# Kernel tuning notes

Measured on AMD Instinct MI355X. Metric: run time of the kernel, lower is better.

## Reference

```python
import jax, jax.numpy as jnp
import numpy as np
from jax.scipy.special import i0

# NUFFT adjoint (gridding) configuration, matching m_op.plan(uv, (256,256), (512,512), (6,6))
N = 256          # image side
K = 512
J = 6            # kernel support per dim
B = 8            # batch
M = 100000       # n_measurements
ALPHA = K / N    # oversampling = 2
BETA = float(np.pi * np.sqrt((J / ALPHA * (ALPHA - 0.5)) ** 2 - 0.8))  # Fessler KB beta


def setup_inputs() -> dict:
    key = jax.random.key(0)
    k1, k2, k3, k4 = jax.random.split(key, 4)
    y_real = jax.random.normal(k1, (B, M), dtype=jnp.float32)
    y_imag = jax.random.normal(k2, (B, M), dtype=jnp.float32)
    weights = jax.random.uniform(k3, (M,), dtype=jnp.float32, minval=0.1, maxval=1.0)
    uv = jax.random.uniform(k4, (M, 2), dtype=jnp.float32,
                            minval=-np.pi, maxval=np.pi)
    return {"y_real": y_real, "y_imag": y_imag, "weights": weights, "uv": uv}


def _kb(t):
    # Kaiser-Bessel interpolation kernel, support |t| <= J/2
    u = 2.0 * t / J
    return i0(BETA * jnp.sqrt(jnp.clip(1.0 - u * u, 0.0))) / i0(jnp.asarray(BETA, jnp.float32))


def reference(y_real, y_imag, weights, uv):
    # weighted complex measurements: inputs * measurement_weights
    y = (y_real + 1j * y_imag) * weights[None, :]           # (B, M) complex64

    # map uv in [-pi, pi) to oversampled grid coords in [0, K)
    kf = uv * (K / (2.0 * np.pi))                            # (M, 2), DC at index 0 (mod K)
    base = jnp.floor(kf).astype(jnp.int32)                   # (M, 2)
    offs = jnp.arange(-J // 2 + 1, J // 2 + 1)               # [-2..3], 6 taps
    idx = base[:, :, None] + offs[None, None, :]             # (M, 2, J)
    dist = idx.astype(jnp.float32) - kf[:, :, None]
    w = _kb(dist)                                            # (M, 2, J) separable weights
    idxm = jnp.mod(idx, K)                                   # wrap onto torus

    w2 = (w[:, 0, :, None] * w[:, 1, None, :]).reshape(M, J * J)          # (M, 36)
    lin = (idxm[:, 0, :, None] * K + idxm[:, 1, None, :]).reshape(M * J * J)
    vals = (y[:, :, None] * w2[None, :, :].astype(jnp.complex64)).reshape(B, M * J * J)

    # scatter-add onto oversampled Fourier grid
    grid = jnp.zeros((B, K * K), jnp.complex64).at[:, lin].add(vals)
    grid = grid.reshape(B, K, K)

    # inverse FFT, center, crop to N x N
    img = jnp.fft.fftshift(jnp.fft.ifft2(grid), axes=(1, 2))
    c = K // 2
    img = img[:, c - N // 2:c + N // 2, c - N // 2:c + N // 2]

    # deapodization: divide by 1D FT of the KB kernel (always real here since BETA > pi*J/4*... )
    n = jnp.arange(N, dtype=jnp.float32) - N // 2
    xf = np.pi * J * n / K
    arg = BETA * BETA - xf * xf
    d = jnp.sinh(jnp.sqrt(arg)) / jnp.sqrt(arg)              # (N,)
    apod = d[:, None] * d[None, :]

    x = (jnp.real(img) / apod).astype(jnp.float32)           # tf.math.real(adj_op(...))

    # per-image min-max rescale
    tmax = jnp.max(x, axis=(1, 2), keepdims=True)
    tmin = jnp.min(x, axis=(1, 2), keepdims=True)
    return (x - tmin) / (tmax - tmin)
```

## Files before the change

### kernel.cpp

```cpp
#include <hip/hip_runtime.h>
#include <math.h>

#define NN 256
#define KK 512
#define JJ 6
#define BB 8
#define MPTS 100000
#define NBINS (KK * KK)
#define KF_SCALE 81.48733086305615f

typedef _Float16 h8 __attribute__((ext_vector_type(8)));
typedef _Float16 h2 __attribute__((ext_vector_type(2)));


__device__ __forceinline__ float i0f_dev(float x) {
    float ax = fabsf(x);
    if (ax < 3.75f) {
        float t = x / 3.75f; t *= t;
        return 1.0f + t*(3.5156229f + t*(3.0899424f + t*(1.2067492f +
               t*(0.2659732f + t*(0.0360768f + t*0.0045813f)))));
    } else {
        float t = 3.75f / ax;
        return (expf(ax) * rsqrtf(ax)) *
               (0.39894228f + t*(0.01328592f + t*(0.00225319f + t*(-0.00157565f +
                t*(0.00916281f + t*(-0.02057706f + t*(0.02635537f +
                t*(-0.01647633f + t*0.00392377f))))))));
    }
}

__device__ __forceinline__ float kbf(float t, float beta, float inv_i0b) {
    float u = t * (1.0f / 3.0f);
    float q = fmaxf(1.0f - u * u, 0.0f);
    return i0f_dev(beta * sqrtf(q)) * inv_i0b;
}

__device__ __forceinline__ int wave_scan(int x, int lane) {
#pragma unroll
    for (int off = 1; off < 64; off <<= 1) {
        int y = __shfl_up(x, off, 64);
        if (lane >= off) x += y;
    }
    return x;
}

__device__ __forceinline__ float kb_lut(const float* __restrict__ sT, float t) {
    float u = (t + 3.0f) * (1023.0f / 6.0f);
    int i = (int)u;
    i = min(i, 1022);
    float f = u - (float)i;
    float a = sT[i];
    return a + f * (sT[i + 1] - sT[i]);
}

__device__ __forceinline__ void tw_lookup(const float* __restrict__ twc,
                                          const float* __restrict__ tws,
                                          int idx, float& wr, float& wi) {
    float sg = (idx & 256) ? -1.0f : 1.0f;
    int ib = idx & 255;
    wr = sg * twc[ib];
    wi = sg * tws[ib];
}


__device__ __forceinline__ void fill_point(
    const float2* __restrict__ uv2,
    const float* __restrict__ y_real, const float* __restrict__ y_imag,
    const float* __restrict__ weights, const int* __restrict__ offsets,
    int* counts, char* rec, const float* sT, int m)
{
    float2 u = uv2[m];
    float kf0 = u.x * KF_SCALE;
    float kf1 = u.y * KF_SCALE;
    float f0 = floorf(kf0), f1 = floorf(kf1);
    float fr0 = kf0 - f0, fr1 = kf1 - f1;
    int b1c = (int)f1 & (KK - 1);
    int bin = (((int)f0 & (KK - 1)) << 9) | b1c;
    int old = atomicSub(&counts[bin], 1);
    int slot = offsets[bin] + old - 1;

    _Float16 hw[12];
#pragma unroll
    for (int j = 0; j < JJ; ++j) {
        hw[j]     = (_Float16)kb_lut(sT, (float)(j - 2) - fr0);
        hw[6 + j] = (_Float16)kb_lut(sT, (float)(j - 2) - fr1);
    }

    float4 c0v, c1v;
    _Float16* p0 = (_Float16*)&c0v;
    _Float16* p1 = (_Float16*)&c1v;
#pragma unroll
    for (int j = 0; j < 8; ++j) p0[j] = hw[j];
#pragma unroll
    for (int j = 0; j < 4; ++j) p1[j] = hw[8 + j];
    ((int*)&c1v)[2] = b1c;
    ((int*)&c1v)[3] = 0;

    float wm = weights[m];
    h8 ha, hb;
#pragma unroll
    for (int b = 0; b < 4; ++b) {
        ha[2 * b]     = (_Float16)(y_real[b * MPTS + m] * wm);
        ha[2 * b + 1] = (_Float16)(y_imag[b * MPTS + m] * wm);
        hb[2 * b]     = (_Float16)(y_real[(b + 4) * MPTS + m] * wm);
        hb[2 * b + 1] = (_Float16)(y_imag[(b + 4) * MPTS + m] * wm);
    }

    float4* dst = (float4*)(rec + (size_t)slot * 64);
    dst[0] = c0v;
    dst[1] = c1v;
    dst[2] = *(float4*)&ha;
    dst[3] = *(float4*)&hb;
}

__device__ __forceinline__ void gather_strip(
    const int* __restrict__ offsets, const char* __restrict__ rec,
    h2* __restrict__ gridh, char* myl, int j, int w, int lane)
{
    int half = lane >> 5;
    int l32 = lane & 31;
    int xcd = j & 7;
    int c0 = (xcd << 6) + ((j >> 3) & 63);
    int q4 = j >> 9;
    int c1base = (q4 << 7) + (w << 5);
    int c1 = c1base + l32;
    int wa = c1 - 3, wb = c1 + 2;

    float aR[4], aI[4];
#pragma unroll
    for (int b = 0; b < 4; ++b) { aR[b] = 0.0f; aI[b] = 0.0f; }

    for (int j0 = 0; j0 < JJ; ++j0) {
        int r0 = (c0 - (j0 - 2)) & (KK - 1);
        int rowbase = r0 << 9;
        int lo = c1base - 3, hi = c1base + 33;
        int nseg, ga0, gb0, ga1, gb1;
        if (lo < 0)        { ga0 = lo; gb0 = -1;  ga1 = 0;   gb1 = hi; nseg = 2; }
        else if (hi > 511) { ga0 = lo; gb0 = 511; ga1 = 512; gb1 = hi; nseg = 2; }
        else               { ga0 = lo; gb0 = hi;  ga1 = 0;   gb1 = 0;  nseg = 1; }

        for (int sgi = 0; sgi < nseg; ++sgi) {
            int ga = sgi ? ga1 : ga0;
            int gb = sgi ? gb1 : gb0;
            int pstart = offsets[rowbase + (ga & 511)];
            int pend   = offsets[rowbase + ((gb & 511) + 1)];
            int ia = max(wa, ga), ib = min(wb, gb);
            bool has = ia <= ib;
            int pA = has ? offsets[rowbase + (ia & 511)] : 0;
            int pB = has ? ((ib == gb) ? pend
                                       : offsets[rowbase + ((ib + 1) & 511)]) : 0;

            for (int pc = pstart; pc < pend; pc += 32) {
                int cnt = min(32, pend - pc);
                int sub = lane & 3;
                int prow = lane >> 2;
#pragma unroll
                for (int qq = 0; qq < 2; ++qq) {
                    if (16 * qq < cnt) {
                        int pp = min(pc + prow + 16 * qq, MPTS - 1);
                        float4 v = *(const float4*)(rec + (size_t)pp * 64 + sub * 16);
                        *(float4*)(myl + (prow + 16 * qq) * 88 + sub * 16) = v;
                    }
                }
                int pLo = max(pA, pc), pHi = min(pB, pc + cnt);
                for (int p = pLo; p < pHi; ++p) {
                    const char* rp = myl + (p - pc) * 88;
                    int bin1 = *(const int*)(rp + 24);
                    int idx = (c1 - bin1 + 2) & 511;
                    bool ok = idx <= 5;
                    idx = ok ? idx : 0;
                    float w0 = (float)*(const _Float16*)(rp + j0 * 2);
                    float w1 = (float)*(const _Float16*)(rp + 12 + idx * 2);
                    float ww = ok ? w0 * w1 : 0.0f;
                    h8 yv = *(const h8*)(rp + 32 + (half << 4));
#pragma unroll
                    for (int b = 0; b < 4; ++b) {
                        aR[b] += (float)yv[2 * b]     * ww;
                        aI[b] += (float)yv[2 * b + 1] * ww;
                    }
                }
            }
        }
    }

    int c = (c0 << 9) + c1;
#pragma unroll
    for (int b = 0; b < 4; ++b) {
        h2 v;
        v[0] = (_Float16)aR[b];
        v[1] = (_Float16)aI[b];
        gridh[((size_t)((half << 2) + b) << 18) + c] = v;
    }
}

__device__ __forceinline__ void wave_fft512(float xr[8], float xi[8], int lane,
                                            const float* __restrict__ twc,
                                            const float* __restrict__ tws)
{
    float a0r = xr[0]+xr[4], a0i = xi[0]+xi[4];
    float a4r = xr[0]-xr[4], a4i = xi[0]-xi[4];
    float a2r = xr[2]+xr[6], a2i = xi[2]+xi[6];
    float a6r = xr[2]-xr[6], a6i = xi[2]-xi[6];
    float a1r = xr[1]+xr[5], a1i = xi[1]+xi[5];
    float a5r = xr[1]-xr[5], a5i = xi[1]-xi[5];
    float a3r = xr[3]+xr[7], a3i = xi[3]+xi[7];
    float a7r = xr[3]-xr[7], a7i = xi[3]-xi[7];
    float b0r = a0r+a2r, b0i = a0i+a2i;
    float b2r = a0r-a2r, b2i = a0i-a2i;
    float b4r = a4r-a6i, b4i = a4i+a6r;
    float b6r = a4r+a6i, b6i = a4i-a6r;
    float b1r = a1r+a3r, b1i = a1i+a3i;
    float b3r = a1r-a3r, b3i = a1i-a3i;
    float b5r = a5r-a7i, b5i = a5i+a7r;
    float b7r = a5r+a7i, b7i = a5i-a7r;
    const float S2 = 0.70710678118654752f;
    float w5r = S2*(b5r-b5i), w5i = S2*(b5r+b5i);
    float w7r = -S2*(b7r+b7i), w7i = S2*(b7r-b7i);
    float y1r = b4r+w5r, y1i = b4i+w5i;
    float y5r = b4r-w5r, y5i = b4i-w5i;
    float y2r = b2r-b3i, y2i = b2i+b3r;
    float y6r = b2r+b3i, y6i = b2i-b3r;
    float y3r = b6r+w7r, y3i = b6i+w7i;
    float y7r = b6r-w7r, y7i = b6i-w7i;

    int p = __brev((unsigned)lane) >> 26;
    xr[0] = b0r+b1r; xi[0] = b0i+b1i;
    {
        float wr, wi;
        tw_lookup(twc, tws, p,     wr, wi); xr[1] = y1r*wr - y1i*wi; xi[1] = y1i*wr + y1r*wi;
        tw_lookup(twc, tws, p * 2, wr, wi); xr[2] = y2r*wr - y2i*wi; xi[2] = y2i*wr + y2r*wi;
        tw_lookup(twc, tws, p * 3, wr, wi); xr[3] = y3r*wr - y3i*wi; xi[3] = y3i*wr + y3r*wi;
        float y4r = b0r-b1r, y4i = b0i-b1i;
        tw_lookup(twc, tws, p * 4, wr, wi); xr[4] = y4r*wr - y4i*wi; xi[4] = y4i*wr + y4r*wi;
        tw_lookup(twc, tws, p * 5, wr, wi); xr[5] = y5r*wr - y5i*wi; xi[5] = y5i*wr + y5r*wi;
        tw_lookup(twc, tws, p * 6, wr, wi); xr[6] = y6r*wr - y6i*wi; xi[6] = y6i*wr + y6r*wi;
        tw_lookup(twc, tws, p * 7, wr, wi); xr[7] = y7r*wr - y7i*wi; xi[7] = y7i*wr + y7r*wi;
    }

#pragma unroll
    for (int t = 0; t < 6; ++t) {
        int m = 1 << t;
        int j = lane & (m - 1);
        int ti = j << (8 - t);
        float wc = twc[ti], wsn = tws[ti];
        bool hi = (lane & m) != 0;
#pragma unroll
        for (int d = 0; d < 8; ++d) {
            float pR = __shfl_xor(xr[d], m, 64);
            float pI = __shfl_xor(xi[d], m, 64);
            float bR = hi ? xr[d] : pR;
            float bI = hi ? xi[d] : pI;
            float aR = hi ? pR : xr[d];
            float aI = hi ? pI : xi[d];
            float wbR = wc * bR - wsn * bI;
            float wbI = wc * bI + wsn * bR;
            xr[d] = hi ? aR - wbR : aR + wbR;
            xi[d] = hi ? aI - wbI : aI + wbI;
        }
    }
}

__device__ __forceinline__ void wave_fft256(float xr[4], float xi[4], int lane,
                                            const float* __restrict__ twc,
                                            const float* __restrict__ tws)
{
    float t0r = xr[0]+xr[2], t0i = xi[0]+xi[2];
    float t1r = xr[0]-xr[2], t1i = xi[0]-xi[2];
    float t2r = xr[1]+xr[3], t2i = xi[1]+xi[3];
    float t3r = xr[1]-xr[3], t3i = xi[1]-xi[3];
    float y1r = t1r-t3i, y1i = t1i+t3r;
    float y3r = t1r+t3i, y3i = t1i-t3r;

    int p2 = (__brev((unsigned)lane) >> 26) << 1;
    xr[0] = t0r+t2r; xi[0] = t0i+t2i;
    {
        float wr, wi;
        tw_lookup(twc, tws, p2,     wr, wi); xr[1] = y1r*wr - y1i*wi; xi[1] = y1i*wr + y1r*wi;
        float y2r = t0r-t2r, y2i = t0i-t2i;
        tw_lookup(twc, tws, p2 * 2, wr, wi); xr[2] = y2r*wr - y2i*wi; xi[2] = y2i*wr + y2r*wi;
        tw_lookup(twc, tws, p2 * 3, wr, wi); xr[3] = y3r*wr - y3i*wi; xi[3] = y3i*wr + y3r*wi;
    }

#pragma unroll
    for (int t = 0; t < 6; ++t) {
        int m = 1 << t;
        int j = lane & (m - 1);
        int ti = j << (8 - t);
        float wc = twc[ti], wsn = tws[ti];
        bool hi = (lane & m) != 0;
#pragma unroll
        for (int d = 0; d < 4; ++d) {
            float pR = __shfl_xor(xr[d], m, 64);
            float pI = __shfl_xor(xi[d], m, 64);
            float bR = hi ? xr[d] : pR;
            float bI = hi ? xi[d] : pI;
            float aR = hi ? pR : xr[d];
            float aI = hi ? pI : xi[d];
            float wbR = wc * bR - wsn * bI;
            float wbI = wc * bI + wsn * bR;
            xr[d] = hi ? aR - wbR : aR + wbR;
            xi[d] = hi ? aI - wbI : aI + wbI;
        }
    }
}

__device__ __forceinline__ void fftA_body(const h2* __restrict__ gridh,
                                          h2* __restrict__ Ch, int bx, int t,
                                          float* sR, float* sI,
                                          float* twc, float* tws)
{
    int lane = t & 63;
    int w = t >> 6;
    int x  = bx & 7;
    int b  = (bx >> 3) & 7;
    int k1base = (x << 6) | (((bx >> 6) & 7) << 3);
    int k1 = k1base + w;

    if (t < 256) {
        float ang = (float)(2.0 * M_PI / 512.0) * (float)t;
        float s, c; sincosf(ang, &s, &c);
        twc[t] = c; tws[t] = s;
    }

    const h2* row = gridh + ((size_t)b << 18) + ((size_t)k1 << 9);
    int p = __brev((unsigned)lane) >> 26;
    float xr[8], xi[8];
#pragma unroll
    for (int a = 0; a < 8; ++a) {
        h2 v = row[p + (a << 6)];
        xr[a] = (float)v[0]; xi[a] = (float)v[1];
    }
    __syncthreads();

    wave_fft512(xr, xi, lane, twc, tws);

    bool act = (lane < 16) | (lane >= 48);
    int lpp = (lane < 16) ? lane : (lane - 32);
    if (act) {
#pragma unroll
        for (int d = 0; d < 8; ++d) {
            int addr = w * 264 + d * 33 + lpp;
            sR[addr] = xr[d];
            sI[addr] = xi[d];
        }
    }
    __syncthreads();

#pragma unroll
    for (int pp = 0; pp < 4; ++pp) {
        int idx = pp * 512 + t;
        int kk = idx & 7;
        int s2 = idx >> 3;
        int v = (s2 + 128) & 255;
        int d = v & 7;
        int lp = v >> 3;
        int addr = kk * 264 + d * 33 + lp;
        h2 o;
        o[0] = (_Float16)sR[addr];
        o[1] = (_Float16)sI[addr];
        Ch[(((size_t)(b << 8) + s2) << 9) + k1base + kk] = o;
    }
}

__device__ __forceinline__ void fftB_body(const h2* __restrict__ Ch,
                                          float* __restrict__ imgT, float beta2,
                                          float* __restrict__ pmin,
                                          float* __restrict__ pmax,
                                          int bx, int t,
                                          float* twc, float* tws, float* invd,
                                          float (*wor)[256], float* wmn, float* wmx)
{
    int lane = t & 63;
    int w = t >> 6;
    int row = w >> 1;
    int odd = w & 1;
    int rowid = bx * 4 + row;
    int b = rowid >> 8;
    int s2 = rowid & 255;

    if (t < 256) {
        float ang = (float)(2.0 * M_PI / 512.0) * (float)t;
        float s, c; sincosf(ang, &s, &c);
        twc[t] = c; tws[t] = s;
    } else if (t < 512) {
        int i = t - 256;
        const float XF = (float)(M_PI * (double)JJ / (double)KK);
        float n = (float)(i - 128);
        float xf = XF * n;
        float arg = beta2 - xf * xf;
        float sq = sqrtf(arg);
        invd[i] = sq / sinhf(sq);
    }

    const h2* rowp = Ch + ((size_t)rowid << 9);
    int p = __brev((unsigned)lane) >> 26;
    float xr[4], xi[4];
#pragma unroll
    for (int a = 0; a < 4; ++a) {
        h2 v = rowp[((p + (a << 6)) << 1) | odd];
        xr[a] = (float)v[0]; xi[a] = (float)v[1];
    }
    __syncthreads();

    wave_fft256(xr, xi, lane, twc, tws);

    if (odd) {
        float4 wo;
#pragma unroll
        for (int d = 0; d < 4; ++d) {
            int k = (lane << 2) + d;
            ((float*)&wo)[d] = xr[d] * twc[k] - xi[d] * tws[k];
        }
        *(float4*)&wor[row][lane << 2] = wo;
    }
    __syncthreads();

    if (!odd) {
        const float INVK2 = 1.0f / ((float)KK * (float)KK);
        float sbase = INVK2 * invd[s2];
        float lmin = 1e30f, lmax = -1e30f;
        float4 wo = *(const float4*)&wor[row][lane << 2];
        float vals[4];
#pragma unroll
        for (int d = 0; d < 4; ++d) {
            int k = (lane << 2) + d;
            float e = xr[d];
            float woK = ((const float*)&wo)[d];
            float xre = (k < 128) ? (e + woK) : (e - woK);
            int r = (k + 128) & 255;
            float o = xre * sbase * invd[r];
            vals[d] = o;
            lmin = fminf(lmin, o);
            lmax = fmaxf(lmax, o);
        }
        int r0run = ((lane << 2) + 128) & 255;
        *(float4*)(imgT + ((size_t)b << 16) + (s2 << 8) + r0run) =
            make_float4(vals[0], vals[1], vals[2], vals[3]);
#pragma unroll
        for (int off = 32; off >= 1; off >>= 1) {
            lmin = fminf(lmin, __shfl_xor(lmin, off, 64));
            lmax = fmaxf(lmax, __shfl_xor(lmax, off, 64));
        }
        if (lane == 0) { wmn[row] = lmin; wmx[row] = lmax; }
    }
    __syncthreads();
    if (t == 0) {
        float mn = fminf(fminf(wmn[0], wmn[1]), fminf(wmn[2], wmn[3]));
        float mx = fmaxf(fmaxf(wmx[0], wmx[1]), fmaxf(wmx[2], wmx[3]));
        pmin[bx] = mn;
        pmax[bx] = mx;
    }
}

__device__ __forceinline__ void norm_body(const float* __restrict__ imgT,
                                          const float* __restrict__ pmin,
                                          const float* __restrict__ pmax,
                                          float* __restrict__ out,
                                          int bx, int t, int nthr,
                                          float (*tile)[65], float* s_mn, float* s_inv)
{
    int b = bx >> 4;
    int tl = bx & 15;
    int r0 = (tl & 3) << 6;
    int s0 = (tl >> 2) << 6;
    int tr = t & 63;
    int ts = t >> 6;
    int nts = nthr >> 6;

    if (t < 64) {
        float mn = pmin[(b << 6) + t];
        float mx = pmax[(b << 6) + t];
#pragma unroll
        for (int off = 32; off >= 1; off >>= 1) {
            mn = fminf(mn, __shfl_xor(mn, off, 64));
            mx = fmaxf(mx, __shfl_xor(mx, off, 64));
        }
        if (t == 0) { *s_mn = mn; *s_inv = 1.0f / (mx - mn); }
    }

    const float* src = imgT + ((size_t)b << 16);
    for (int s2i = ts; s2i < 64; s2i += nts)
        tile[s2i][tr] = src[((s0 + s2i) << 8) + r0 + tr];
    __syncthreads();

    float mn = *s_mn, inv = *s_inv;
    float* dst = out + ((size_t)b << 16);
    for (int ri = ts; ri < 64; ri += nts)
        dst[((r0 + ri) << 8) + s0 + tr] = (tile[tr][ri] - mn) * inv;
}


__global__ __launch_bounds__(256) void count_bins(
    const float2* __restrict__ uv2, int* __restrict__ counts,
    float* __restrict__ lut, float beta, float inv_i0b)
{
    int m = blockIdx.x * 256 + threadIdx.x;
    if (m < 1024) {
        float t = -3.0f + (6.0f / 1023.0f) * (float)m;
        lut[m] = kbf(t, beta, inv_i0b);
    }
    if (m >= MPTS) return;
    float2 u = uv2[m];
    int b0 = (int)floorf(u.x * KF_SCALE) & (KK - 1);
    int b1 = (int)floorf(u.y * KF_SCALE) & (KK - 1);
    atomicAdd(&counts[(b0 << 9) | b1], 1);
}

__global__ __launch_bounds__(1024) void scan_k(
    const int* __restrict__ counts, int* __restrict__ offsets,
    unsigned long long* __restrict__ desc)
{
    __shared__ int part[16];
    __shared__ int s_prefix;
    int tid = threadIdx.x;
    int lane = tid & 63;
    int w = tid >> 6;
    int g = blockIdx.x * 1024 + tid;

    int v = counts[g];
    int x = wave_scan(v, lane);
    if (lane == 63) part[w] = x;
    __syncthreads();
    if (tid < 16) {
        int p = part[tid];
#pragma unroll
        for (int off = 1; off < 16; off <<= 1) {
            int y = __shfl_up(p, off, 64);
            if (tid >= off) p += y;
        }
        part[tid] = p;
    }
    __syncthreads();
    int incl = x + ((w > 0) ? part[w - 1] : 0);
    int total = part[15];

    if (tid == 0) {
        unsigned long long pack = ((unsigned long long)(unsigned)total << 2) |
                                  ((blockIdx.x == 0) ? 2ULL : 1ULL);
        atomicExch(&desc[blockIdx.x], pack);
        if (blockIdx.x == 0) s_prefix = 0;
    }

    if (blockIdx.x > 0 && w == 0) {
        int prefix = 0;
        int base = blockIdx.x - 1;
        bool done = false;
        while (!done) {
            int idx = base - lane;
            unsigned long long d = 0;
            if (idx >= 0) {
                do { d = atomicAdd(&desc[idx], 0ULL); } while ((d & 3ULL) == 0ULL);
            }
            unsigned long long mask = __ballot(idx >= 0 && (d & 3ULL) == 2ULL);
            int f = (mask != 0ULL) ? (__ffsll((long long)mask) - 1) : 64;
            int contrib = (idx >= 0 && lane <= f) ? (int)(d >> 2) : 0;
#pragma unroll
            for (int off = 1; off < 64; off <<= 1)
                contrib += __shfl_xor(contrib, off, 64);
            prefix += contrib;
            base -= 64;
            done = (mask != 0ULL);
        }
        if (lane == 0) {
            s_prefix = prefix;
            atomicExch(&desc[blockIdx.x],
                       ((unsigned long long)(unsigned)(prefix + total) << 2) | 2ULL);
        }
    }
    __syncthreads();

    offsets[g] = incl - v + s_prefix;
    if (g == 0) offsets[NBINS] = MPTS;
}

__global__ __launch_bounds__(256) void fill_records(
    const float2* __restrict__ uv2,
    const float* __restrict__ y_real, const float* __restrict__ y_imag,
    const float* __restrict__ weights, const int* __restrict__ offsets,
    int* __restrict__ counts, char* __restrict__ rec,
    const float* __restrict__ lut)
{
    __shared__ float sT[1024];
    int tid = threadIdx.x;
#pragma unroll
    for (int q = 0; q < 4; ++q) sT[q * 256 + tid] = lut[q * 256 + tid];
    __syncthreads();
    int m = blockIdx.x * 256 + tid;
    if (m >= MPTS) return;
    fill_point(uv2, y_real, y_imag, weights, offsets, counts, rec, sT, m);
}

__global__ __launch_bounds__(256) void gather_grid(
    const int* __restrict__ offsets, const char* __restrict__ rec,
    h2* __restrict__ gridh)
{
    __shared__ __align__(16) char lds[4][2816];
    int t = threadIdx.x;
    gather_strip(offsets, rec, gridh, lds[t >> 6], blockIdx.x, t >> 6, t & 63);
}

__global__ __launch_bounds__(512) void fftA(
    const h2* __restrict__ gridh, h2* __restrict__ Ch)
{
    __shared__ float sR[2112], sI[2112];
    __shared__ float twc[256], tws[256];
    fftA_body(gridh, Ch, blockIdx.x, threadIdx.x, sR, sI, twc, tws);
}

__global__ __launch_bounds__(512) void fftB(
    const h2* __restrict__ Ch, float* __restrict__ imgT, float beta2,
    float* __restrict__ pmin, float* __restrict__ pmax)
{
    __shared__ float twc[256], tws[256];
    __shared__ float invd[256];
    __shared__ __align__(16) float wor[4][256];
    __shared__ float wmn[4], wmx[4];
    fftB_body(Ch, imgT, beta2, pmin, pmax, blockIdx.x, threadIdx.x,
              twc, tws, invd, wor, wmn, wmx);
}

__global__ __launch_bounds__(256) void norm_t(
    const float* __restrict__ imgT, const float* __restrict__ pmin,
    const float* __restrict__ pmax, float* __restrict__ out)
{
    __shared__ float tile[64][65];
    __shared__ float s_mn, s_inv;
    norm_body(imgT, pmin, pmax, out, blockIdx.x, threadIdx.x, 256,
              tile, &s_mn, &s_inv);
}


static double i0_host(double x) {
    double sum = 1.0, term = 1.0;
    double q = x * x * 0.25;
    for (int k = 1; k < 80; ++k) {
        term *= q / ((double)k * (double)k);
        sum += term;
        if (term < sum * 1e-17) break;
    }
    return sum;
}

extern "C" void kernel_launch(void* const* d_in, const int* in_sizes, int n_in,
                              void* d_out, int out_size, void* d_ws, size_t ws_size,
                              hipStream_t stream)
{
    const float* y_real  = (const float*)d_in[0];
    const float* y_imag  = (const float*)d_in[1];
    const float* weights = (const float*)d_in[2];
    const float2* uv2    = (const float2*)d_in[3];
    float* out = (float*)d_out;

    char* W = (char*)d_ws;
    h2*       gridh   = (h2*)W;
    int*      counts  = (int*)W;
    unsigned long long* desc = (unsigned long long*)(W + 0x100000);
    float*    imgT    = (float*)W;
    char*     A       = W + (size_t)16 * 1024 * 1024;
    char*     rec     = A;
    int*      offsets = (int*)(A + 6400000);
    h2*       Ch      = (h2*)A;
    float*    pmin    = (float*)(A + 8400000);
    float*    pmax    = (float*)(A + 8402048);
    float*    lut     = (float*)(A + 8404096);

    double beta_d = M_PI * sqrt(19.45);
    float beta = (float)beta_d;
    float inv_i0b = (float)(1.0 / i0_host(beta_d));
    float beta2 = (float)(beta_d * beta_d);

    hipMemsetAsync(counts, 0, NBINS * sizeof(int) + 256 * sizeof(unsigned long long),
                   stream);

    count_bins<<<(MPTS + 255) / 256, 256, 0, stream>>>(
        uv2, counts, lut, beta, inv_i0b);

    scan_k<<<256, 1024, 0, stream>>>(counts, offsets, desc);

    fill_records<<<(MPTS + 255) / 256, 256, 0, stream>>>(
        uv2, y_real, y_imag, weights, offsets, counts, rec, lut);

    gather_grid<<<2048, 256, 0, stream>>>(offsets, rec, gridh);

    fftA<<<512, 512, 0, stream>>>(gridh, Ch);

    fftB<<<512, 512, 0, stream>>>(Ch, imgT, beta2, pmin, pmax);

    norm_t<<<128, 256, 0, stream>>>(imgT, pmin, pmax, out);
}
```

Before: 139.1 us.

## Replace decoupled look-back scan with two-pass block-totals scan

The single-pass scan with look-back descriptor spinning is replaced by two kernels. The first writes per-block exclusive scans and block totals. The second rescans the 512 block totals in every block and adds the block prefix to its offsets. This removes the serial spin-wait chain across blocks and the descriptor memset. In exchange it adds one kernel launch and an extra read-modify-write pass over the 1 MB offsets array.

Measured after the change: 138.0 us. About the same (-0.8%).

```diff
diff --git a/kernel.cpp b/kernel.cpp
--- a/kernel.cpp
+++ b/kernel.cpp
@@ -505,71 +505,65 @@
     atomicAdd(&counts[(b0 << 9) | b1], 1);
 }
 
-__global__ __launch_bounds__(1024) void scan_k(
+__global__ __launch_bounds__(512) void scan_a(
     const int* __restrict__ counts, int* __restrict__ offsets,
-    unsigned long long* __restrict__ desc)
-{
-    __shared__ int part[16];
-    __shared__ int s_prefix;
-    int tid = threadIdx.x;
-    int lane = tid & 63;
-    int w = tid >> 6;
-    int g = blockIdx.x * 1024 + tid;
-
-    int v = counts[g];
+    int* __restrict__ btot)
+{
+    __shared__ int part[8];
+    int t = threadIdx.x;
+    int lane = t & 63;
+    int w8 = t >> 6;
+    int gid = blockIdx.x * 512 + t;
+
+    int v = counts[gid];
     int x = wave_scan(v, lane);
-    if (lane == 63) part[w] = x;
-    __syncthreads();
-    if (tid < 16) {
-        int p = part[tid];
-#pragma unroll
-        for (int off = 1; off < 16; off <<= 1) {
-            int y = __shfl_up(p, off, 64);
-            if (tid >= off) p += y;
-        }
-        part[tid] = p;
-    }
-    __syncthreads();
-    int incl = x + ((w > 0) ? part[w - 1] : 0);
-    int total = part[15];
-
-    if (tid == 0) {
-        unsigned long long pack = ((unsigned long long)(unsigned)total << 2) |
-                                  ((blockIdx.x == 0) ? 2ULL : 1ULL);
-        atomicExch(&desc[blockIdx.x], pack);
-        if (blockIdx.x == 0) s_prefix = 0;
-    }
-
-    if (blockIdx.x > 0 && w == 0) {
-        int prefix = 0;
-        int base = blockIdx.x - 1;
-        bool done = false;
-        while (!done) {
-            int idx = base - lane;
-            unsigned long long d = 0;
-            if (idx >= 0) {
-                do { d = atomicAdd(&desc[idx], 0ULL); } while ((d & 3ULL) == 0ULL);
-            }
-            unsigned long long mask = __ballot(idx >= 0 && (d & 3ULL) == 2ULL);
-            int f = (mask != 0ULL) ? (__ffsll((long long)mask) - 1) : 64;
-            int contrib = (idx >= 0 && lane <= f) ? (int)(d >> 2) : 0;
-#pragma unroll
-            for (int off = 1; off < 64; off <<= 1)
-                contrib += __shfl_xor(contrib, off, 64);
-            prefix += contrib;
-            base -= 64;
-            done = (mask != 0ULL);
-        }
-        if (lane == 0) {
-            s_prefix = prefix;
-            atomicExch(&desc[blockIdx.x],
-                       ((unsigned long long)(unsigned)(prefix + total) << 2) | 2ULL);
-        }
-    }
-    __syncthreads();
-
-    offsets[g] = incl - v + s_prefix;
-    if (g == 0) offsets[NBINS] = MPTS;
+    if (lane == 63) part[w8] = x;
+    __syncthreads();
+    if (t < 8) {
+        int pq = part[t];
+#pragma unroll
+        for (int off = 1; off < 8; off <<= 1) {
+            int y = __shfl_up(pq, off, 64);
+            if (t >= off) pq += y;
+        }
+        part[t] = pq;
+    }
+    __syncthreads();
+    int incl = x + ((w8 > 0) ? part[w8 - 1] : 0);
+    offsets[gid] = incl - v;
+    if (t == 511) btot[blockIdx.x] = incl;
+}
+
+__global__ __launch_bounds__(512) void scan_b(
+    int* __restrict__ offsets, const int* __restrict__ btot)
+{
+    __shared__ int part[8];
+    __shared__ int s_pref;
+    int t = threadIdx.x;
+    int lane = t & 63;
+    int w8 = t >> 6;
+
+    int v = btot[t];
+    int x = wave_scan(v, lane);
+    if (lane == 63) part[w8] = x;
+    __syncthreads();
+    if (t < 8) {
+        int pq = part[t];
+#pragma unroll
+        for (int off = 1; off < 8; off <<= 1) {
+            int y = __shfl_up(pq, off, 64);
+            if (t >= off) pq += y;
+        }
+        part[t] = pq;
+    }
+    __syncthreads();
+    int incl = x + ((w8 > 0) ? part[w8 - 1] : 0);
+    if (t == blockIdx.x) s_pref = incl - v;
+    __syncthreads();
+
+    int gid = blockIdx.x * 512 + t;
+    offsets[gid] += s_pref;
+    if (gid == 0) offsets[NBINS] = MPTS;
 }
 
 __global__ __launch_bounds__(256) void fill_records(
@@ -653,7 +647,7 @@
     char* W = (char*)d_ws;
     h2*       gridh   = (h2*)W;
     int*      counts  = (int*)W;
-    unsigned long long* desc = (unsigned long long*)(W + 0x100000);
+    int*      btot    = (int*)(W + 0x100000);
     float*    imgT    = (float*)W;
     char*     A       = W + (size_t)16 * 1024 * 1024;
     char*     rec     = A;
@@ -668,13 +662,13 @@
     float inv_i0b = (float)(1.0 / i0_host(beta_d));
     float beta2 = (float)(beta_d * beta_d);
 
-    hipMemsetAsync(counts, 0, NBINS * sizeof(int) + 256 * sizeof(unsigned long long),
-                   stream);
+    hipMemsetAsync(counts, 0, NBINS * sizeof(int), stream);
 
     count_bins<<<(MPTS + 255) / 256, 256, 0, stream>>>(
         uv2, counts, lut, beta, inv_i0b);
 
-    scan_k<<<256, 1024, 0, stream>>>(counts, offsets, desc);
+    scan_a<<<512, 512, 0, stream>>>(counts, offsets, btot);
+    scan_b<<<512, 512, 0, stream>>>(offsets, btot);
 
     fill_records<<<(MPTS + 255) / 256, 256, 0, stream>>>(
         uv2, y_real, y_imag, weights, offsets, counts, rec, lut);
```
